# Kernel tuning notes

Hardware: AMD Instinct MI355X
Metric: run time of the kernel (lower is better)

The kernel has to match this reference:

```python
import jax, jax.numpy as jnp
import numpy as np
from jax import lax

B, N, C, T = 1024, 128, 3, 100
H = 128  # lstm hidden / feature size

def setup_inputs() -> dict:
    key = jax.random.key(0)
    ks = jax.random.split(key, 12)
    s = 0.05
    return {
        'x': jax.random.normal(ks[0], (B, N, C, T), jnp.float32),
        'conv_w': jax.random.normal(ks[1], (64, 3, 5), jnp.float32) * s,
        'conv_b': jax.random.normal(ks[2], (64,), jnp.float32) * s,
        'w_ih': jax.random.normal(ks[3], (4 * H, 64), jnp.float32) * s,
        'w_hh': jax.random.normal(ks[4], (4 * H, H), jnp.float32) * s,
        'b_ih': jax.random.normal(ks[5], (4 * H,), jnp.float32) * s,
        'b_hh': jax.random.normal(ks[6], (4 * H,), jnp.float32) * s,
        'W1': jax.random.normal(ks[7], (H, 2 * H), jnp.float32) * s,
        'W2': jax.random.normal(ks[8], (H, H), jnp.float32) * s,
        'W0': jax.random.normal(ks[9], (H, H), jnp.float32) * s,
        'ln_g': jnp.ones((H,), jnp.float32),
        'ln_b': jnp.zeros((H,), jnp.float32),
        'lin_w': jax.random.normal(ks[10], (H, H), jnp.float32) * s,
        'lin_b': jax.random.normal(ks[11], (H,), jnp.float32) * s,
    }

def _forward(x, conv_w, conv_b, w_ih, w_hh, b_ih, b_hh, W1, W2, W0, ln_g, ln_b, lin_w, lin_b):
    b, n = x.shape[0], x.shape[1]
    # --- agent encode: conv1d(3->64, k=5, pad=2) + relu on x[:,0] ---
    agent = x[:, 0]  # [B,3,T]
    h = lax.conv_general_dilated(agent, conv_w, (1,), [(2, 2)],
                                 dimension_numbers=('NCH', 'OIH', 'NCH'))
    h = jax.nn.relu(h + conv_b[None, :, None])  # [B,64,T]
    seq = jnp.transpose(h, (2, 0, 1))  # [T,B,64]
    # --- single-layer LSTM (pytorch gate order i,f,g,o) ---
    bias = b_ih + b_hh
    def step(carry, xt):
        hp, cp = carry
        gates = xt @ w_ih.T + hp @ w_hh.T + bias  # [B,4H]
        i, f, g, o = jnp.split(gates, 4, axis=-1)
        c = jax.nn.sigmoid(f) * cp + jax.nn.sigmoid(i) * jnp.tanh(g)
        hn = jax.nn.sigmoid(o) * jnp.tanh(c)
        return (hn, c), None
    init = (jnp.zeros((b, H), x.dtype), jnp.zeros((b, H), x.dtype))
    (agent_out, _), _ = lax.scan(step, init, seq)  # agent_out: [B,128]
    # NOTE: original code appends agent_out for ALL N slots (its loop bug);
    # faithful: all_vehicle_out = agent_out repeated N times.
    all_out = jnp.broadcast_to(agent_out[:, None, :], (b, n, H))  # [B,N,128]
    # --- Attention: res = W0 x0 + sum_i W2 tanh(W1 [x0; xi]) (vectorized) ---
    x0 = all_out[:, 0]           # [B,128]
    others = all_out[:, 1:]      # [B,N-1,128]
    x0b = jnp.broadcast_to(x0[:, None, :], others.shape)
    cat = jnp.concatenate([x0b, others], axis=-1)       # [B,N-1,256]
    inter = jnp.tanh(jnp.einsum('bnf,hf->bnh', cat, W1))
    inter = jnp.einsum('bnh,fh->bnf', inter, W2)        # [B,N-1,128]
    res = x0 @ W0.T + inter.sum(axis=1)                 # [B,128]
    # --- layernorm(128) ---
    mu = res.mean(-1, keepdims=True)
    var = ((res - mu) ** 2).mean(-1, keepdims=True)
    res = (res - mu) * lax.rsqrt(var + 1e-5) * ln_g + ln_b
    # --- linear(128,128) then repeat to [B,14,14,128] ---
    res = res @ lin_w.T + lin_b
    return jnp.tile(res[:, None, None, :], (1, 14, 14, 1))

def reference(x, conv_w, conv_b, w_ih, w_hh, b_ih, b_hh, W1, W2, W0, ln_g, ln_b, lin_w, lin_b):
    return _forward(x, conv_w, conv_b, w_ih, w_hh, b_ih, b_hh, W1, W2, W0, ln_g, ln_b, lin_w, lin_b)
```

## Files before the change

### kernel.cpp

```cpp
#include <hip/hip_runtime.h>
#include <math.h>


#define T_STEPS 100
#define LROW    208
#define PLANE   (16 * LROW)

#define OFF_WHI    0u
#define OFF_BIAS   393216u
#define OFF_W1CT   395264u
#define OFF_W2T    460800u
#define OFF_W0T    526336u
#define OFF_LINWT  591872u
#define OFF_XHI    657408u
#define OFF_HFIN   26871808u

typedef __attribute__((ext_vector_type(8))) _Float16 half8;
typedef __attribute__((ext_vector_type(4))) float f32x4;

__device__ __forceinline__ float frcp(float x) { return __builtin_amdgcn_rcpf(x); }
__device__ __forceinline__ float fexp2(float x) { return __builtin_amdgcn_exp2f(x); }
__device__ __forceinline__ float tanhf_fast(float x) { return 2.f * frcp(1.f + __expf(-2.f * x)) - 1.f; }

__global__ void prep_kernel(const float* __restrict__ w_ih, const float* __restrict__ w_hh,
                            const float* __restrict__ b_ih, const float* __restrict__ b_hh,
                            const float* __restrict__ W1, const float* __restrict__ W2,
                            const float* __restrict__ W0, const float* __restrict__ lin_w,
                            char* __restrict__ wsb) {
    _Float16* whi  = (_Float16*)(wsb + OFF_WHI);
    float*  biasv = (float*)(wsb + OFF_BIAS);
    float*  W1cT  = (float*)(wsb + OFF_W1CT);
    float*  W2T   = (float*)(wsb + OFF_W2T);
    float*  W0T   = (float*)(wsb + OFF_W0T);
    float*  linWT = (float*)(wsb + OFF_LINWT);

    const float fold[4] = {-1.4426950408889634f, -1.4426950408889634f,
                           -2.8853900817779268f, -1.4426950408889634f};

    int blk = blockIdx.x, tid = threadIdx.x;
    if (blk < 192) {
        int idx = blk * 512 + tid;
        int e = idx & 7;
        int l = (idx >> 3) & 63;
        int s = (idx >> 9) & 3;
        int rem = idx >> 11;
        int kt = rem % 6, w = rem / 6;
        int g = s * 128 + 16 * w + (l & 15);
        int k = kt * 32 + (l >> 4) * 8 + e;
        float v = (k < 64) ? w_ih[g * 64 + k] : w_hh[g * 128 + (k - 64)];
        whi[idx] = (_Float16)(v * fold[s]);
    } else if (blk == 192) {
        int s = tid >> 7;
        biasv[tid] = (b_ih[tid] + b_hh[tid]) * fold[s];
    } else if (blk < 225) {
        int idx = (blk - 193) * 512 + tid;
        int f = idx >> 7, hh = idx & 127;
        W1cT[f * 128 + hh] = W1[hh * 256 + f] + W1[hh * 256 + 128 + f];
    } else if (blk < 257) {
        int idx = (blk - 225) * 512 + tid;
        int h = idx >> 7, f = idx & 127;
        W2T[h * 128 + f] = W2[f * 128 + h];
    } else if (blk < 289) {
        int idx = (blk - 257) * 512 + tid;
        int k = idx >> 7, f = idx & 127;
        W0T[k * 128 + f] = W0[f * 128 + k];
    } else {
        int idx = (blk - 289) * 512 + tid;
        int k = idx >> 7, f = idx & 127;
        linWT[k * 128 + f] = lin_w[f * 128 + k];
    }
}

__global__ __launch_bounds__(256) void conv_kernel(const float* __restrict__ x,
                                                   const float* __restrict__ conv_w,
                                                   const float* __restrict__ conv_b,
                                                   char* __restrict__ wsb) {
    _Float16* xhi = (_Float16*)(wsb + OFF_XHI);
    __shared__ float sx[3][104];
    __shared__ float sw[960];
    __shared__ float sb[64];
    int b = blockIdx.x, tid = threadIdx.x;

    for (int i = tid; i < 312; i += 256) {
        int c = i / 104, tp = i % 104;
        int t = tp - 2;
        sx[c][tp] = (t >= 0 && t < 100) ? x[b * 38400 + c * 100 + t] : 0.f;
    }
    for (int i = tid; i < 960; i += 256) sw[i] = conv_w[i];
    if (tid < 64) sb[tid] = conv_b[tid];
    __syncthreads();

    for (int i = tid; i < 6400; i += 256) {
        int t = i >> 6, k = i & 63;
        float a = sb[k];
#pragma unroll
        for (int c = 0; c < 3; ++c)
#pragma unroll
            for (int kk = 0; kk < 5; ++kk)
                a += sx[c][t + kk] * sw[k * 15 + c * 5 + kk];
        a = fmaxf(a, 0.f);
        xhi[t * 65536 + b * 64 + k] = (_Float16)a;
    }
}

__global__ __launch_bounds__(512, 2)
void lstm_mfma(const char* __restrict__ wsro, char* __restrict__ wsb) {
    const _Float16* whi  = (const _Float16*)(wsro + OFF_WHI);
    const float*  biasv  = (const float*)(wsro + OFF_BIAS);
    const _Float16* xhi  = (const _Float16*)(wsro + OFF_XHI);
    float* hfin = (float*)(wsb + OFF_HFIN);

    __shared__ _Float16 L[2][16][LROW];

    int tid = threadIdx.x;
    int w = tid >> 6, l = tid & 63;
    int b0 = blockIdx.x * 16;

    half8 wx[2][4];
    half8 wh[4][4];
#pragma unroll
    for (int ktx = 0; ktx < 2; ++ktx)
#pragma unroll
        for (int s = 0; s < 4; ++s)
            wx[ktx][s] = *(const half8*)(whi + (((w * 6 + ktx) * 4 + s) * 64 + l) * 8);
#pragma unroll
    for (int kth = 0; kth < 4; ++kth)
#pragma unroll
        for (int s = 0; s < 4; ++s)
            wh[kth][s] = *(const half8*)(whi + (((w * 6 + 2 + kth) * 4 + s) * 64 + l) * 8);

    int jl = 16 * w + (l & 15);
    float bv[4];
#pragma unroll
    for (int s = 0; s < 4; ++s) bv[s] = biasv[s * 128 + jl];

    int arow = l & 15;
    int g16  = (l >> 4) * 16;
    uint rowbase = (uint)arow * (LROW * 2);
    uint rswz    = (uint)(arow & 7) << 4;
    int hrow0 = (l >> 4) * 4;

    int xr = tid >> 5;
    uint xw = ((uint)xr * (LROW * 2) + (uint)(tid & 31) * 4) ^ ((uint)(xr & 7) << 4);

    uint hwa[4];
#pragma unroll
    for (int r = 0; r < 4; ++r) {
        uint row = (uint)(hrow0 + r);
        hwa[r] = (row * (LROW * 2) + 128u + 2u * (uint)jl) ^ ((row & 7u) << 4);
    }

    float cst[4]  = {0.f, 0.f, 0.f, 0.f};
    float hreg[4] = {0.f, 0.f, 0.f, 0.f};

    for (int i = tid; i < 2 * PLANE; i += 512) ((_Float16*)L)[i] = (_Float16)0.f;

    size_t xoff0 = (size_t)b0 * 64 + (size_t)tid * 2;
    uint vx = *(const uint*)(xhi + xoff0);
    __syncthreads();
    *(uint*)((char*)&L[0][0][0] + xw) = vx;
    vx = *(const uint*)(xhi + xoff0 + 65536);
    __syncthreads();

    for (int t = 0; t < T_STEPS; ++t) {
        int p = t & 1;
        const char* ph = (const char*)&L[p][0][0];
        char* qh = (char*)&L[p ^ 1][0][0];

        if (t < T_STEPS - 1) {
            *(uint*)(qh + xw) = vx;
            int tn = (t + 2 < T_STEPS) ? t + 2 : T_STEPS - 1;
            vx = *(const uint*)(xhi + xoff0 + (size_t)tn * 65536);
        }

        f32x4 accA[4], accB[4];
#pragma unroll
        for (int s = 0; s < 4; ++s) {
            accA[s] = (f32x4){bv[s], bv[s], bv[s], bv[s]};
            accB[s] = (f32x4){0.f, 0.f, 0.f, 0.f};
        }

#pragma unroll
        for (int ktx = 0; ktx < 2; ++ktx) {
            half8 ax = *(const half8*)(ph + ((rowbase + (uint)ktx * 64 + g16) ^ rswz));
#pragma unroll
            for (int s = 0; s < 4; ++s)
                accA[s] = __builtin_amdgcn_mfma_f32_16x16x32_f16(ax, wx[ktx][s], accA[s], 0, 0, 0);
        }
#pragma unroll
        for (int kth = 0; kth < 2; ++kth) {
            half8 ah = *(const half8*)(ph + ((rowbase + 128u + (uint)kth * 64 + g16) ^ rswz));
#pragma unroll
            for (int s = 0; s < 4; ++s)
                accA[s] = __builtin_amdgcn_mfma_f32_16x16x32_f16(ah, wh[kth][s], accA[s], 0, 0, 0);
        }
#pragma unroll
        for (int kth = 2; kth < 4; ++kth) {
            half8 ah = *(const half8*)(ph + ((rowbase + 128u + (uint)kth * 64 + g16) ^ rswz));
#pragma unroll
            for (int s = 0; s < 4; ++s)
                accB[s] = __builtin_amdgcn_mfma_f32_16x16x32_f16(ah, wh[kth][s], accB[s], 0, 0, 0);
        }

#pragma unroll
        for (int r = 0; r < 4; ++r) {
            float Ei = fexp2(accA[0][r] + accB[0][r]);
            float Ef = fexp2(accA[1][r] + accB[1][r]);
            float Eg = fexp2(accA[2][r] + accB[2][r]);
            float Eo = fexp2(accA[3][r] + accB[3][r]);
            float si = frcp(1.f + Ei);
            float sf = frcp(1.f + Ef);
            float tg = 2.f * frcp(1.f + Eg) - 1.f;
            float so = frcp(1.f + Eo);
            cst[r] = sf * cst[r] + si * tg;
            float tc = 2.f * frcp(1.f + fexp2(cst[r] * -2.8853900817779268f)) - 1.f;
            hreg[r] = so * tc;
        }

        if (t < T_STEPS - 1) {
#pragma unroll
            for (int r = 0; r < 4; ++r)
                *(_Float16*)(qh + hwa[r]) = (_Float16)hreg[r];
            __syncthreads();
        }
    }

#pragma unroll
    for (int r = 0; r < 4; ++r)
        hfin[(size_t)(b0 + hrow0 + r) * 128 + jl] = hreg[r];
}

__global__ __launch_bounds__(128) void post_kernel(const char* __restrict__ wsb,
                                                   const float* __restrict__ ln_g,
                                                   const float* __restrict__ ln_b,
                                                   const float* __restrict__ lin_b,
                                                   float* __restrict__ out) {
    const float* hfinal = (const float*)(wsb + OFF_HFIN);
    const float* W1cT   = (const float*)(wsb + OFF_W1CT);
    const float* W2T    = (const float*)(wsb + OFF_W2T);
    const float* W0T    = (const float*)(wsb + OFF_W0T);
    const float* linWT  = (const float*)(wsb + OFF_LINWT);

    __shared__ float sh[128], su[128], sres[128], so_[128], spart[4];
    int b = blockIdx.x, f = threadIdx.x;

    sh[f] = hfinal[(size_t)b * 128 + f];
    __syncthreads();

    float acc = 0.f;
#pragma unroll 4
    for (int k = 0; k < 128; ++k) acc += W1cT[k * 128 + f] * sh[k];
    su[f] = tanhf_fast(acc);
    __syncthreads();

    float v = 0.f, r0 = 0.f;
#pragma unroll 4
    for (int k = 0; k < 128; ++k) {
        v  += W2T[k * 128 + f] * su[k];
        r0 += W0T[k * 128 + f] * sh[k];
    }
    float res = r0 + 127.f * v;

    int lane = f & 63, wid = f >> 6;
    float s = res;
#pragma unroll
    for (int off = 32; off > 0; off >>= 1) s += __shfl_down(s, off);
    if (lane == 0) spart[wid] = s;
    __syncthreads();
    float mu = (spart[0] + spart[1]) * (1.f / 128.f);
    float d = res - mu;
    float s2 = d * d;
#pragma unroll
    for (int off = 32; off > 0; off >>= 1) s2 += __shfl_down(s2, off);
    if (lane == 0) spart[2 + wid] = s2;
    __syncthreads();
    float var = (spart[2] + spart[3]) * (1.f / 128.f);
    float rn = d * rsqrtf(var + 1e-5f) * ln_g[f] + ln_b[f];
    sres[f] = rn;
    __syncthreads();

    float o = lin_b[f];
#pragma unroll 4
    for (int k = 0; k < 128; ++k) o += linWT[k * 128 + f] * sres[k];
    so_[f] = o;
    __syncthreads();

    float4 val = *(const float4*)&so_[(f & 31) << 2];
    float4* op4 = (float4*)(out + (size_t)b * 25088);
#pragma unroll 7
    for (int i = 0; i < 49; ++i) op4[i * 128 + f] = val;
}

extern "C" void kernel_launch(void* const* d_in, const int* in_sizes, int n_in,
                              void* d_out, int out_size, void* d_ws, size_t ws_size,
                              hipStream_t stream) {
    const float* x      = (const float*)d_in[0];
    const float* conv_w = (const float*)d_in[1];
    const float* conv_b = (const float*)d_in[2];
    const float* w_ih   = (const float*)d_in[3];
    const float* w_hh   = (const float*)d_in[4];
    const float* b_ih   = (const float*)d_in[5];
    const float* b_hh   = (const float*)d_in[6];
    const float* W1     = (const float*)d_in[7];
    const float* W2     = (const float*)d_in[8];
    const float* W0     = (const float*)d_in[9];
    const float* ln_g   = (const float*)d_in[10];
    const float* ln_b   = (const float*)d_in[11];
    const float* lin_w  = (const float*)d_in[12];
    const float* lin_b  = (const float*)d_in[13];
    char* wsb  = (char*)d_ws;
    float* out = (float*)d_out;

    prep_kernel<<<dim3(321), dim3(512), 0, stream>>>(w_ih, w_hh, b_ih, b_hh,
                                                     W1, W2, W0, lin_w, wsb);
    conv_kernel<<<dim3(1024), dim3(256), 0, stream>>>(x, conv_w, conv_b, wsb);
    lstm_mfma<<<dim3(64), dim3(512), 0, stream>>>(wsb, wsb);
    post_kernel<<<dim3(1024), dim3(128), 0, stream>>>(wsb, ln_g, ln_b, lin_b, out);
}
```

Before: 159.7 us.

## Fuse prep and conv kernels, chain MFMAs, and merge LSTM gate reciprocals

Merges the weight-prep and conv kernels into a single launch so one kernel boundary goes away. In the LSTM step, all six A-fragment LDS loads are issued up front and the MFMAs form one chain that starts from the bias vector, replacing the two accumulators that had to be added afterwards. The gate math combines pairs of reciprocals into one, e.g. sigmoid(i)*tanh(g) computed as (1-Eg)/((1+Ei)(1+Eg)), which cuts transcendental ops on the serial critical path. The products in the combined reciprocals can overflow to inf for large gate pre-activations, and the single MFMA chain is longer in dependency depth.

```diff
diff --git a/kernel.cpp b/kernel.cpp
--- a/kernel.cpp
+++ b/kernel.cpp
@@ -22,17 +22,26 @@
 __device__ __forceinline__ float fexp2(float x) { return __builtin_amdgcn_exp2f(x); }
 __device__ __forceinline__ float tanhf_fast(float x) { return 2.f * frcp(1.f + __expf(-2.f * x)) - 1.f; }
 
-__global__ void prep_kernel(const float* __restrict__ w_ih, const float* __restrict__ w_hh,
-                            const float* __restrict__ b_ih, const float* __restrict__ b_hh,
-                            const float* __restrict__ W1, const float* __restrict__ W2,
-                            const float* __restrict__ W0, const float* __restrict__ lin_w,
-                            char* __restrict__ wsb) {
+#define MF16(A, B, C) __builtin_amdgcn_mfma_f32_16x16x32_f16((A), (B), (C), 0, 0, 0)
+
+__global__ __launch_bounds__(512)
+void prep_conv_kernel(const float* __restrict__ w_ih, const float* __restrict__ w_hh,
+                      const float* __restrict__ b_ih, const float* __restrict__ b_hh,
+                      const float* __restrict__ W1, const float* __restrict__ W2,
+                      const float* __restrict__ W0, const float* __restrict__ lin_w,
+                      const float* __restrict__ x, const float* __restrict__ conv_w,
+                      const float* __restrict__ conv_b, char* __restrict__ wsb) {
+    __shared__ float sx[3][104];
+    __shared__ float sw[960];
+    __shared__ float sb[64];
+
     _Float16* whi  = (_Float16*)(wsb + OFF_WHI);
     float*  biasv = (float*)(wsb + OFF_BIAS);
     float*  W1cT  = (float*)(wsb + OFF_W1CT);
     float*  W2T   = (float*)(wsb + OFF_W2T);
     float*  W0T   = (float*)(wsb + OFF_W0T);
     float*  linWT = (float*)(wsb + OFF_LINWT);
+    _Float16* xhi = (_Float16*)(wsb + OFF_XHI);
 
     const float fold[4] = {-1.4426950408889634f, -1.4426950408889634f,
                            -2.8853900817779268f, -1.4426950408889634f};
@@ -64,42 +73,32 @@
         int idx = (blk - 257) * 512 + tid;
         int k = idx >> 7, f = idx & 127;
         W0T[k * 128 + f] = W0[f * 128 + k];
-    } else {
+    } else if (blk < 321) {
         int idx = (blk - 289) * 512 + tid;
         int k = idx >> 7, f = idx & 127;
         linWT[k * 128 + f] = lin_w[f * 128 + k];
-    }
-}
-
-__global__ __launch_bounds__(256) void conv_kernel(const float* __restrict__ x,
-                                                   const float* __restrict__ conv_w,
-                                                   const float* __restrict__ conv_b,
-                                                   char* __restrict__ wsb) {
-    _Float16* xhi = (_Float16*)(wsb + OFF_XHI);
-    __shared__ float sx[3][104];
-    __shared__ float sw[960];
-    __shared__ float sb[64];
-    int b = blockIdx.x, tid = threadIdx.x;
-
-    for (int i = tid; i < 312; i += 256) {
-        int c = i / 104, tp = i % 104;
-        int t = tp - 2;
-        sx[c][tp] = (t >= 0 && t < 100) ? x[b * 38400 + c * 100 + t] : 0.f;
-    }
-    for (int i = tid; i < 960; i += 256) sw[i] = conv_w[i];
-    if (tid < 64) sb[tid] = conv_b[tid];
-    __syncthreads();
-
-    for (int i = tid; i < 6400; i += 256) {
-        int t = i >> 6, k = i & 63;
-        float a = sb[k];
-#pragma unroll
-        for (int c = 0; c < 3; ++c)
-#pragma unroll
-            for (int kk = 0; kk < 5; ++kk)
-                a += sx[c][t + kk] * sw[k * 15 + c * 5 + kk];
-        a = fmaxf(a, 0.f);
-        xhi[t * 65536 + b * 64 + k] = (_Float16)a;
+    } else {
+        int b = blk - 321;
+        for (int i = tid; i < 312; i += 512) {
+            int c = i / 104, tp = i % 104;
+            int t = tp - 2;
+            sx[c][tp] = (t >= 0 && t < 100) ? x[b * 38400 + c * 100 + t] : 0.f;
+        }
+        for (int i = tid; i < 960; i += 512) sw[i] = conv_w[i];
+        if (tid < 64) sb[tid] = conv_b[tid];
+        __syncthreads();
+
+        for (int i = tid; i < 6400; i += 512) {
+            int t = i >> 6, k = i & 63;
+            float a = sb[k];
+#pragma unroll
+            for (int c = 0; c < 3; ++c)
+#pragma unroll
+                for (int kk = 0; kk < 5; ++kk)
+                    a += sx[c][t + kk] * sw[k * 15 + c * 5 + kk];
+            a = fmaxf(a, 0.f);
+            xhi[t * 65536 + b * 64 + k] = (_Float16)a;
+        }
     }
 }
 
@@ -130,9 +129,12 @@
             wh[kth][s] = *(const half8*)(whi + (((w * 6 + 2 + kth) * 4 + s) * 64 + l) * 8);
 
     int jl = 16 * w + (l & 15);
-    float bv[4];
-#pragma unroll
-    for (int s = 0; s < 4; ++s) bv[s] = biasv[s * 128 + jl];
+    f32x4 bvec[4];
+#pragma unroll
+    for (int s = 0; s < 4; ++s) {
+        float bv = biasv[s * 128 + jl];
+        bvec[s] = (f32x4){bv, bv, bv, bv};
+    }
 
     int arow = l & 15;
     int g16  = (l >> 4) * 16;
@@ -173,48 +175,39 @@
             vx = *(const uint*)(xhi + xoff0 + (size_t)tn * 65536);
         }
 
-        f32x4 accA[4], accB[4];
-#pragma unroll
-        for (int s = 0; s < 4; ++s) {
-            accA[s] = (f32x4){bv[s], bv[s], bv[s], bv[s]};
-            accB[s] = (f32x4){0.f, 0.f, 0.f, 0.f};
-        }
-
-#pragma unroll
-        for (int ktx = 0; ktx < 2; ++ktx) {
-            half8 ax = *(const half8*)(ph + ((rowbase + (uint)ktx * 64 + g16) ^ rswz));
-#pragma unroll
-            for (int s = 0; s < 4; ++s)
-                accA[s] = __builtin_amdgcn_mfma_f32_16x16x32_f16(ax, wx[ktx][s], accA[s], 0, 0, 0);
-        }
-#pragma unroll
-        for (int kth = 0; kth < 2; ++kth) {
-            half8 ah = *(const half8*)(ph + ((rowbase + 128u + (uint)kth * 64 + g16) ^ rswz));
-#pragma unroll
-            for (int s = 0; s < 4; ++s)
-                accA[s] = __builtin_amdgcn_mfma_f32_16x16x32_f16(ah, wh[kth][s], accA[s], 0, 0, 0);
-        }
-#pragma unroll
-        for (int kth = 2; kth < 4; ++kth) {
-            half8 ah = *(const half8*)(ph + ((rowbase + 128u + (uint)kth * 64 + g16) ^ rswz));
-#pragma unroll
-            for (int s = 0; s < 4; ++s)
-                accB[s] = __builtin_amdgcn_mfma_f32_16x16x32_f16(ah, wh[kth][s], accB[s], 0, 0, 0);
-        }
+        half8 ax0 = *(const half8*)(ph + ((rowbase + 0u   + g16) ^ rswz));
+        half8 ax1 = *(const half8*)(ph + ((rowbase + 64u  + g16) ^ rswz));
+        half8 ah0 = *(const half8*)(ph + ((rowbase + 128u + g16) ^ rswz));
+        half8 ah1 = *(const half8*)(ph + ((rowbase + 192u + g16) ^ rswz));
+        half8 ah2 = *(const half8*)(ph + ((rowbase + 256u + g16) ^ rswz));
+        half8 ah3 = *(const half8*)(ph + ((rowbase + 320u + g16) ^ rswz));
+
+        f32x4 acc[4];
+#pragma unroll
+        for (int s = 0; s < 4; ++s) acc[s] = MF16(ax0, wx[0][s], bvec[s]);
+#pragma unroll
+        for (int s = 0; s < 4; ++s) acc[s] = MF16(ax1, wx[1][s], acc[s]);
+#pragma unroll
+        for (int s = 0; s < 4; ++s) acc[s] = MF16(ah0, wh[0][s], acc[s]);
+#pragma unroll
+        for (int s = 0; s < 4; ++s) acc[s] = MF16(ah1, wh[1][s], acc[s]);
+#pragma unroll
+        for (int s = 0; s < 4; ++s) acc[s] = MF16(ah2, wh[2][s], acc[s]);
+#pragma unroll
+        for (int s = 0; s < 4; ++s) acc[s] = MF16(ah3, wh[3][s], acc[s]);
 
 #pragma unroll
         for (int r = 0; r < 4; ++r) {
-            float Ei = fexp2(accA[0][r] + accB[0][r]);
-            float Ef = fexp2(accA[1][r] + accB[1][r]);
-            float Eg = fexp2(accA[2][r] + accB[2][r]);
-            float Eo = fexp2(accA[3][r] + accB[3][r]);
-            float si = frcp(1.f + Ei);
-            float sf = frcp(1.f + Ef);
-            float tg = 2.f * frcp(1.f + Eg) - 1.f;
-            float so = frcp(1.f + Eo);
-            cst[r] = sf * cst[r] + si * tg;
-            float tc = 2.f * frcp(1.f + fexp2(cst[r] * -2.8853900817779268f)) - 1.f;
-            hreg[r] = so * tc;
+            float Ei = fexp2(acc[0][r]);
+            float Ef = fexp2(acc[1][r]);
+            float Eg = fexp2(acc[2][r]);
+            float Eo = fexp2(acc[3][r]);
+            float rf  = frcp(1.f + Ef);
+            float rig = frcp((1.f + Ei) * (1.f + Eg));
+            cst[r] = rf * cst[r] + (1.f - Eg) * rig;
+            float Ec = fexp2(cst[r] * -2.8853900817779268f);
+            float roc = frcp((1.f + Eo) * (1.f + Ec));
+            hreg[r] = (1.f - Ec) * roc;
         }
 
         if (t < T_STEPS - 1) {
@@ -311,9 +304,9 @@
     char* wsb  = (char*)d_ws;
     float* out = (float*)d_out;
 
-    prep_kernel<<<dim3(321), dim3(512), 0, stream>>>(w_ih, w_hh, b_ih, b_hh,
-                                                     W1, W2, W0, lin_w, wsb);
-    conv_kernel<<<dim3(1024), dim3(256), 0, stream>>>(x, conv_w, conv_b, wsb);
+    prep_conv_kernel<<<dim3(1345), dim3(512), 0, stream>>>(w_ih, w_hh, b_ih, b_hh,
+                                                           W1, W2, W0, lin_w,
+                                                           x, conv_w, conv_b, wsb);
     lstm_mfma<<<dim3(64), dim3(512), 0, stream>>>(wsb, wsb);
     post_kernel<<<dim3(1024), dim3(128), 0, stream>>>(wsb, ln_g, ln_b, lin_b, out);
 }
```

Result: faster. 148.4 us (-7.1%).
